# Optimization experiments

Measured on AMD Instinct MI355X. Metric: run time of the kernel, lower is better.

Reference implementation:

```python
import jax, jax.numpy as jnp
import numpy as np

N_EMBD = 1024
N_HEAD = 16
HEAD_DIM = N_EMBD // N_HEAD
WINDOW = 256
STRIDE = 128
GLOBAL = 16


def build_sparse_causal_mask(t):
    i = jnp.arange(t)[:, None]
    j = jnp.arange(t)[None, :]
    causal = j <= i
    allowed = causal & ((i - j) < WINDOW)
    allowed = allowed | (((i - j) % STRIDE == 0) & causal)
    allowed = allowed | ((j < GLOBAL) & causal)
    return allowed  # [t, t] bool


def setup_inputs() -> dict:
    key = jax.random.key(0)
    k1, k2, k3, k4, k5 = jax.random.split(key, 5)
    b, t = 2, 4096
    s = 1.0 / np.sqrt(N_EMBD)
    return {
        "x": jax.random.normal(k1, (b, t, N_EMBD), dtype=jnp.float32),
        "w_qkv": jax.random.normal(k2, (N_EMBD, 3 * N_EMBD), dtype=jnp.float32) * s,
        "b_qkv": jnp.zeros((3 * N_EMBD,), dtype=jnp.float32),
        "w_proj": jax.random.normal(k3, (N_EMBD, N_EMBD), dtype=jnp.float32) * s,
        "b_proj": jnp.zeros((N_EMBD,), dtype=jnp.float32),
    }


def reference(x, w_qkv, b_qkv, w_proj, b_proj):
    b, t, c = x.shape
    qkv = x @ w_qkv + b_qkv  # [b, t, 3c]
    q, k, v = jnp.split(qkv, 3, axis=2)
    # [b, h, t, d]
    q = q.reshape(b, t, N_HEAD, HEAD_DIM).transpose(0, 2, 1, 3)
    k = k.reshape(b, t, N_HEAD, HEAD_DIM).transpose(0, 2, 1, 3)
    v = v.reshape(b, t, N_HEAD, HEAD_DIM).transpose(0, 2, 1, 3)

    allowed = build_sparse_causal_mask(t)  # [t, t]
    scale = 1.0 / np.sqrt(HEAD_DIM)
    att = jnp.einsum("bhqd,bhkd->bhqk", q, k) * scale
    att = jnp.where(allowed, att, -jnp.inf)
    att = jax.nn.softmax(att, axis=-1)
    y = jnp.einsum("bhqk,bhkd->bhqd", att, v)
    y = y.transpose(0, 2, 1, 3).reshape(b, t, c)
    return y @ w_proj + b_proj
```

## Files before the change

kernel.cpp:

```cpp
#include <hip/hip_runtime.h>
#include <hip/hip_bf16.h>
#include <stdint.h>

typedef unsigned short ushort_t;
typedef __attribute__((ext_vector_type(8))) __bf16 bf16x8;
typedef __attribute__((ext_vector_type(8))) short short8;
typedef __attribute__((ext_vector_type(4))) float f32x4;
typedef __attribute__((ext_vector_type(4))) unsigned int uint4v;

__device__ __forceinline__ ushort_t f2b(float f) {
  union { float f; uint32_t u; } c; c.f = f;
  return (ushort_t)((c.u + 0x7fffu + ((c.u >> 16) & 1u)) >> 16);
}
__device__ __forceinline__ float b2f(ushort_t b) {
  union { float f; uint32_t u; } c; c.u = ((uint32_t)b) << 16;
  return c.f;
}
__device__ __forceinline__ float dot2bf(uint32_t qu, uint32_t ku, float acc) {
  union { uint32_t u; float f; } a, b, c, d;
  a.u = qu << 16; b.u = qu & 0xffff0000u;
  c.u = ku << 16; d.u = ku & 0xffff0000u;
  acc = fmaf(a.f, c.f, acc);
  return fmaf(b.f, d.f, acc);
}

__global__ __launch_bounds__(256) void f32_to_b16(
    const float* __restrict__ in, ushort_t* __restrict__ out) {
  const int i = (blockIdx.x * 256 + threadIdx.x) * 8;
  const f32x4 a = *(const f32x4*)&in[i];
  const f32x4 b = *(const f32x4*)&in[i + 4];
  short8 t;
#pragma unroll
  for (int j = 0; j < 4; j++) { t[j] = (short)f2b(a[j]); t[4 + j] = (short)f2b(b[j]); }
  *(short8*)&out[i] = t;
}

__global__ __launch_bounds__(256) void transpose_f2b(
    const float* __restrict__ in, ushort_t* __restrict__ out, int K, int N) {
  __shared__ __align__(16) ushort_t tile[64][72];
  const int k0 = blockIdx.x * 64, n0 = blockIdx.y * 64;
  const int tid = threadIdx.x;
#pragma unroll
  for (int i = 0; i < 4; i++) {
    const int idx = i * 256 + tid;
    const int r = idx >> 4, c = (idx & 15) * 4;
    const f32x4 a = *(const f32x4*)&in[(size_t)(k0 + r) * N + n0 + c];
#pragma unroll
    for (int j = 0; j < 4; j++) tile[r][c + j] = f2b(a[j]);
  }
  __syncthreads();
#pragma unroll
  for (int i = 0; i < 16; i++) {
    const int idx = i * 256 + tid;
    const int r = idx >> 6, c = idx & 63;
    out[(size_t)(n0 + r) * K + k0 + c] = tile[c][r];
  }
}

template <int MODE>
__global__ __launch_bounds__(256) void gemm_bt(
    const ushort_t* __restrict__ A, const ushort_t* __restrict__ Bt,
    const float* __restrict__ bias,
    ushort_t* __restrict__ q_out, ushort_t* __restrict__ k_out,
    ushort_t* __restrict__ v_out, float* __restrict__ f_out,
    int M, int N, int K) {
  __shared__ __align__(16) ushort_t Als[128 * 64];
  __shared__ __align__(16) ushort_t Bls[128 * 64];
  const int tid = threadIdx.x;
  const int wave = tid >> 6, lane = tid & 63;
  const int quad = lane >> 4, l15 = lane & 15;
  const int wr = wave >> 1, wc = wave & 1;
  const int linear = (int)blockIdx.x + (int)gridDim.x * (int)blockIdx.y;
  const int xcd = linear & 7, chunk = linear >> 3;
  const int by = xcd * 8 + (chunk & 7);
  const int bx = chunk >> 3;
  const int rowBase = by * 128;
  const int colBase = bx * 128;
  const f32x4 fzero = {0.f, 0.f, 0.f, 0.f};

  f32x4 acc[4][4];
#pragma unroll
  for (int mi = 0; mi < 4; mi++)
#pragma unroll
    for (int ni = 0; ni < 4; ni++) acc[mi][ni] = fzero;

  const int srow = tid >> 3;
  const int scol = (tid & 7) * 8;

  for (int kk = 0; kk < K; kk += 64) {
    __syncthreads();
#pragma unroll
    for (int s = 0; s < 4; s++) {
      const int r = s * 32 + srow;
      __builtin_amdgcn_global_load_lds(
          (const __attribute__((address_space(1))) unsigned int*)
              &A[(size_t)(rowBase + r) * K + kk + scol],
          (__attribute__((address_space(3))) unsigned int*)&Als[r * 64 + scol],
          16, 0, 0);
      __builtin_amdgcn_global_load_lds(
          (const __attribute__((address_space(1))) unsigned int*)
              &Bt[(size_t)(colBase + r) * K + kk + scol],
          (__attribute__((address_space(3))) unsigned int*)&Bls[r * 64 + scol],
          16, 0, 0);
    }
    __syncthreads();
#pragma unroll
    for (int ks = 0; ks < 2; ks++) {
      const int ko = ks * 32 + quad * 8;
      bf16x8 af[4], bfr[4];
#pragma unroll
      for (int mi = 0; mi < 4; mi++)
        af[mi] = *(const bf16x8*)&Als[(wr * 64 + mi * 16 + l15) * 64 + ko];
#pragma unroll
      for (int ni = 0; ni < 4; ni++)
        bfr[ni] = *(const bf16x8*)&Bls[(wc * 64 + ni * 16 + l15) * 64 + ko];
#pragma unroll
      for (int mi = 0; mi < 4; mi++)
#pragma unroll
        for (int ni = 0; ni < 4; ni++)
          acc[mi][ni] = __builtin_amdgcn_mfma_f32_16x16x32_bf16(
              af[mi], bfr[ni], acc[mi][ni], 0, 0, 0);
    }
  }

  if (MODE == 0) {
    const int which = colBase >> 10;
    ushort_t* dst = which == 0 ? q_out : (which == 1 ? k_out : v_out);
    const int h = ((colBase & 1023) >> 6) + wc;
#pragma unroll
    for (int mi = 0; mi < 4; mi++) {
#pragma unroll
      for (int ni = 0; ni < 4; ni++) {
        const int d = ni * 16 + l15;
        const float bv = bias[colBase + wc * 64 + d];
#pragma unroll
        for (int r = 0; r < 4; r++) {
          const int row = rowBase + wr * 64 + mi * 16 + quad * 4 + r;
          const int bidx = row >> 12, t = row & 4095;
          dst[(size_t)((bidx * 16 + h) * 4096 + t) * 64 + d] =
              f2b(acc[mi][ni][r] + bv);
        }
      }
    }
  } else {
#pragma unroll
    for (int mi = 0; mi < 4; mi++) {
#pragma unroll
      for (int ni = 0; ni < 4; ni++) {
        const int col = colBase + wc * 64 + ni * 16 + l15;
        const float bv = bias[col];
#pragma unroll
        for (int r = 0; r < 4; r++) {
          const int row = rowBase + wr * 64 + mi * 16 + quad * 4 + r;
          f_out[(size_t)row * N + col] = acc[mi][ni][r] + bv;
        }
      }
    }
  }
}

#define LP 72
__global__ __launch_bounds__(256) void sparse_attn(
    const ushort_t* __restrict__ Qb, const ushort_t* __restrict__ Kb,
    const ushort_t* __restrict__ Vb, ushort_t* __restrict__ Y) {
  __shared__ __align__(16) ushort_t Qls[64 * LP];
  __shared__ __align__(16) char smem[(64 * LP + 64 * LP + 4 * 16 * LP) * 2];
  ushort_t* Kls = (ushort_t*)smem;
  ushort_t* Vtls = Kls + 64 * LP;
  ushort_t* Pls = Vtls + 64 * LP;

  const int tid = threadIdx.x;
  const int wave = tid >> 6, lane = tid & 63;
  const int quad = lane >> 4, l15 = lane & 15;
  const int qt = (int)gridDim.x - 1 - (int)blockIdx.x;
  const int h = blockIdx.y, b = blockIdx.z;
  const int q0 = qt * 64;
  const size_t headoff = (size_t)(b * 16 + h) * 4096 * 64;
  const ushort_t* Qp = Qb + headoff;
  const ushort_t* Kp = Kb + headoff;
  const ushort_t* Vp = Vb + headoff;
  const f32x4 fzero = {0.f, 0.f, 0.f, 0.f};
  const float scale = 0.125f;

#pragma unroll
  for (int i = 0; i < 2; i++) {
    const int idx = i * 256 + tid;
    const int r = idx >> 3, c = (idx & 7) * 8;
    *(short8*)&Qls[r * LP + c] = *(const short8*)&Qp[(size_t)(q0 + r) * 64 + c];
  }
  __syncthreads();
  bf16x8 qf[2];
#pragma unroll
  for (int ks = 0; ks < 2; ks++)
    qf[ks] = *(const bf16x8*)&Qls[(wave * 16 + l15) * LP + ks * 32 + quad * 8];

  f32x4 o[4];
#pragma unroll
  for (int dt = 0; dt < 4; dt++) o[dt] = fzero;
  float mrun[4], lsum[4];
#pragma unroll
  for (int r = 0; r < 4; r++) { mrun[r] = -1e30f; lsum[r] = 0.f; }
  ushort_t* Pw = &Pls[wave * 16 * LP];

  auto dense_tile = [&](int k0, int mode) {
    __syncthreads();
#pragma unroll
    for (int i = 0; i < 2; i++) {
      const int idx = i * 256 + tid;
      const int r = idx >> 3, c = (idx & 7) * 8;
      *(short8*)&Kls[r * LP + c] = *(const short8*)&Kp[(size_t)(k0 + r) * 64 + c];
    }
#pragma unroll
    for (int i = 0; i < 2; i++) {
      const int idx = i * 256 + tid;
      const int key = idx & 63, dblk = (idx >> 6) * 8;
      short8 vv = *(const short8*)&Vp[(size_t)(k0 + key) * 64 + dblk];
#pragma unroll
      for (int m = 0; m < 8; m++) Vtls[(dblk + m) * LP + key] = (ushort_t)vv[m];
    }
    __syncthreads();

    f32x4 sacc[4];
#pragma unroll
    for (int ni = 0; ni < 4; ni++) sacc[ni] = fzero;
#pragma unroll
    for (int ks = 0; ks < 2; ks++) {
      const int ko = ks * 32 + quad * 8;
#pragma unroll
      for (int ni = 0; ni < 4; ni++) {
        bf16x8 kf = *(const bf16x8*)&Kls[(ni * 16 + l15) * LP + ko];
        sacc[ni] = __builtin_amdgcn_mfma_f32_16x16x32_bf16(qf[ks], kf, sacc[ni], 0, 0, 0);
      }
    }

    float p[4][4];
    const int i0 = q0 + wave * 16 + quad * 4;
    if (mode == 0) {
#pragma unroll
      for (int ni = 0; ni < 4; ni++)
#pragma unroll
        for (int r = 0; r < 4; r++) p[ni][r] = sacc[ni][r] * scale;
    } else {
#pragma unroll
      for (int ni = 0; ni < 4; ni++) {
        const int j = k0 + ni * 16 + l15;
#pragma unroll
        for (int r = 0; r < 4; r++) {
          const int dist = i0 + r - j;
          bool ok;
          if (mode == 1)      ok = dist >= 0;
          else if (mode == 2) ok = (dist < 256) || ((dist & 127) == 0);
          else                ok = (dist >= 0) &&
                                   ((dist < 256) || ((dist & 127) == 0) || (j < 16));
          p[ni][r] = ok ? sacc[ni][r] * scale : -1e30f;
        }
      }
    }

    float alpha[4];
#pragma unroll
    for (int r = 0; r < 4; r++) {
      float m = fmaxf(fmaxf(p[0][r], p[1][r]), fmaxf(p[2][r], p[3][r]));
      m = fmaxf(m, __shfl_xor(m, 1));
      m = fmaxf(m, __shfl_xor(m, 2));
      m = fmaxf(m, __shfl_xor(m, 4));
      m = fmaxf(m, __shfl_xor(m, 8));
      const float mnew = fmaxf(mrun[r], m);
      alpha[r] = __expf(mrun[r] - mnew);
      mrun[r] = mnew;
      float rs = 0.f;
#pragma unroll
      for (int ni = 0; ni < 4; ni++) {
        const float e = __expf(p[ni][r] - mnew);
        p[ni][r] = e;
        rs += e;
      }
      rs += __shfl_xor(rs, 1);
      rs += __shfl_xor(rs, 2);
      rs += __shfl_xor(rs, 4);
      rs += __shfl_xor(rs, 8);
      lsum[r] = lsum[r] * alpha[r] + rs;
    }
#pragma unroll
    for (int dt = 0; dt < 4; dt++)
#pragma unroll
      for (int r = 0; r < 4; r++) o[dt][r] *= alpha[r];

#pragma unroll
    for (int ni = 0; ni < 4; ni++)
#pragma unroll
      for (int r = 0; r < 4; r++)
        Pw[(quad * 4 + r) * LP + ni * 16 + l15] = f2b(p[ni][r]);
    __syncthreads();

#pragma unroll
    for (int ks = 0; ks < 2; ks++) {
      const int ko = ks * 32 + quad * 8;
      bf16x8 pf = *(const bf16x8*)&Pw[l15 * LP + ko];
#pragma unroll
      for (int dt = 0; dt < 4; dt++) {
        bf16x8 vf = *(const bf16x8*)&Vtls[(dt * 16 + l15) * LP + ko];
        o[dt] = __builtin_amdgcn_mfma_f32_16x16x32_bf16(pf, vf, o[dt], 0, 0, 0);
      }
    }
  };

  if (qt < 6) {
    for (int kt = 0; kt <= qt; kt++) dense_tile(kt * 64, 3);
  } else {
    dense_tile(0, 3);
    dense_tile((qt - 4) * 64, 2);
    dense_tile((qt - 3) * 64, 0);
    dense_tile((qt - 2) * 64, 0);
    dense_tile((qt - 1) * 64, 0);
    dense_tile(qt * 64, 1);

    const int rowl = wave * 16 + l15;
    const uint4v qv0 = *(const uint4v*)&Qls[rowl * LP + quad * 16];
    const uint4v qv1 = *(const uint4v*)&Qls[rowl * LP + quad * 16 + 8];
    const ushort_t* Kr = Kp + (size_t)rowl * 64 + quad * 16;
    const ushort_t* Vr = Vp + (size_t)rowl * 64 + quad * 16;

    float ms = -1e30f, ls = 0.f;
    f32x4 os4[4];
#pragma unroll
    for (int c = 0; c < 4; c++) os4[c] = fzero;

    auto sproc = [&](uint4v ka0, uint4v ka1, uint4v va0, uint4v va1) {
      float sd = 0.f;
#pragma unroll
      for (int m2 = 0; m2 < 4; m2++) {
        sd = dot2bf(qv0[m2], ka0[m2], sd);
        sd = dot2bf(qv1[m2], ka1[m2], sd);
      }
      sd += __shfl_xor(sd, 16);
      sd += __shfl_xor(sd, 32);
      const float sig = sd * scale;
      const float mnew = fmaxf(ms, sig);
      const float al = __expf(ms - mnew);
      const float e = __expf(sig - mnew);
      ms = mnew;
      ls = ls * al + e;
#pragma unroll
      for (int m2 = 0; m2 < 4; m2++) {
        union { uint32_t u; float f; } va, vb, vc, vd;
        va.u = va0[m2] << 16;
        vb.u = va0[m2] & 0xffff0000u;
        vc.u = va1[m2] << 16;
        vd.u = va1[m2] & 0xffff0000u;
        const int d0 = 2 * m2, d1 = 2 * m2 + 1;
        os4[d0 >> 2][d0 & 3] = fmaf(os4[d0 >> 2][d0 & 3], al, e * va.f);
        os4[d1 >> 2][d1 & 3] = fmaf(os4[d1 >> 2][d1 & 3], al, e * vb.f);
        os4[(d0 + 8) >> 2][d0 & 3] = fmaf(os4[(d0 + 8) >> 2][d0 & 3], al, e * vc.f);
        os4[(d1 + 8) >> 2][d1 & 3] = fmaf(os4[(d1 + 8) >> 2][d1 & 3], al, e * vd.f);
      }
    };

    int k0s = q0 - 384;
    if (k0s >= 64) {
      uint4v ka0 = *(const uint4v*)(Kr + (size_t)k0s * 64);
      uint4v ka1 = *(const uint4v*)(Kr + (size_t)k0s * 64 + 8);
      uint4v va0 = *(const uint4v*)(Vr + (size_t)k0s * 64);
      uint4v va1 = *(const uint4v*)(Vr + (size_t)k0s * 64 + 8);
      while (true) {
        const int nxt = k0s - 128;
        uint4v kb0, kb1, vb0, vb1;
        if (nxt >= 64) {
          kb0 = *(const uint4v*)(Kr + (size_t)nxt * 64);
          kb1 = *(const uint4v*)(Kr + (size_t)nxt * 64 + 8);
          vb0 = *(const uint4v*)(Vr + (size_t)nxt * 64);
          vb1 = *(const uint4v*)(Vr + (size_t)nxt * 64 + 8);
        }
        sproc(ka0, ka1, va0, va1);
        if (nxt < 64) break;
        ka0 = kb0; ka1 = kb1; va0 = vb0; va1 = vb1;
        k0s = nxt;
      }
    }

    __syncthreads();
    float* scr = (float*)smem + wave * (16 * 68);
#pragma unroll
    for (int c = 0; c < 4; c++)
      *(f32x4*)&scr[l15 * 68 + quad * 16 + c * 4] = os4[c];
    asm volatile("s_waitcnt lgkmcnt(0)" ::: "memory");
    __builtin_amdgcn_wave_barrier();
#pragma unroll
    for (int r = 0; r < 4; r++) {
      const float ms_r = __shfl(ms, quad * 4 + r);
      const float ls_r = __shfl(ls, quad * 4 + r);
      const float M = fmaxf(mrun[r], ms_r);
      const float ea = __expf(mrun[r] - M);
      const float eb = __expf(ms_r - M);
      lsum[r] = lsum[r] * ea + ls_r * eb;
#pragma unroll
      for (int dt = 0; dt < 4; dt++)
        o[dt][r] = o[dt][r] * ea + scr[(quad * 4 + r) * 68 + dt * 16 + l15] * eb;
    }
  }

#pragma unroll
  for (int dt = 0; dt < 4; dt++) {
#pragma unroll
    for (int r = 0; r < 4; r++) {
      const int t = q0 + wave * 16 + quad * 4 + r;
      const int c = h * 64 + dt * 16 + l15;
      Y[(size_t)(b * 4096 + t) * 1024 + c] = f2b(o[dt][r] / lsum[r]);
    }
  }
}

static const void* by_size(void* const* d_in, const int* in_sizes, int n_in,
                           int want, int fallback_idx) {
  for (int i = 0; i < n_in; i++)
    if (in_sizes[i] == want) return d_in[i];
  return d_in[fallback_idx];
}

extern "C" void kernel_launch(void* const* d_in, const int* in_sizes, int n_in,
                              void* d_out, int out_size, void* d_ws,
                              size_t ws_size, hipStream_t stream) {
  const float* x      = (const float*)by_size(d_in, in_sizes, n_in, 8388608, 0);
  const float* w_qkv  = (const float*)by_size(d_in, in_sizes, n_in, 3145728, 1);
  const float* b_qkv  = (const float*)by_size(d_in, in_sizes, n_in, 3072, 2);
  const float* w_proj = (const float*)by_size(d_in, in_sizes, n_in, 1048576, 3);
  const float* b_proj = (const float*)by_size(d_in, in_sizes, n_in, 1024, 4);
  float* out = (float*)d_out;
  char* ws = (char*)d_ws;
  ushort_t* wqkvT  = (ushort_t*)(ws);
  ushort_t* wprojT = (ushort_t*)(ws + 6291456);
  ushort_t* qb     = (ushort_t*)(ws + 8388608);
  ushort_t* kb     = (ushort_t*)(ws + 25165824);
  ushort_t* vb     = (ushort_t*)(ws + 41943040);
  ushort_t* yb     = (ushort_t*)(ws + 58720256);
  ushort_t* xb     = yb;

  if (ws_size < 75497472) return;

  f32_to_b16<<<4096, 256, 0, stream>>>(x, xb);
  transpose_f2b<<<dim3(16, 48), 256, 0, stream>>>(w_qkv, wqkvT, 1024, 3072);
  transpose_f2b<<<dim3(16, 16), 256, 0, stream>>>(w_proj, wprojT, 1024, 1024);
  gemm_bt<0><<<dim3(24, 64), 256, 0, stream>>>(
      xb, wqkvT, b_qkv, qb, kb, vb, nullptr, 8192, 3072, 1024);
  sparse_attn<<<dim3(64, 16, 2), 256, 0, stream>>>(qb, kb, vb, yb);
  gemm_bt<1><<<dim3(8, 64), 256, 0, stream>>>(
      yb, wprojT, b_proj, nullptr, nullptr, nullptr, out, 8192, 1024, 1024);
}
```

Before: 343.6 us.

## Process two query tiles per 512-thread block sharing K/V tiles, with XCD-aware mapping

Each attention block now covers two adjacent 64-row query tiles using 8 waves, so every loaded K/V key tile (and its V transpose) in LDS serves both tiles, cutting global and LDS fill traffic. Tiles that only one half needs are skipped per wave group through a mode of -1. Block indices are also remapped so each XCD handles a fixed set of batch-heads, which is meant to improve L2 locality. The trade-offs are a larger LDS footprint, half as many blocks, and some waves sitting idle at barriers on tiles they do not use. The parts of the sparse strided loop that are not shown must also be correct for the new row indexing.

Measured after the change: 302.6 us. -11.9%, faster.

```diff
diff --git a/kernel.cpp b/kernel.cpp
--- a/kernel.cpp
+++ b/kernel.cpp
@@ -160,11 +160,11 @@
 }
 
 #define LP 72
-__global__ __launch_bounds__(256) void sparse_attn(
+__global__ __launch_bounds__(512) void sparse_attn(
     const ushort_t* __restrict__ Qb, const ushort_t* __restrict__ Kb,
     const ushort_t* __restrict__ Vb, ushort_t* __restrict__ Y) {
-  __shared__ __align__(16) ushort_t Qls[64 * LP];
-  __shared__ __align__(16) char smem[(64 * LP + 64 * LP + 4 * 16 * LP) * 2];
+  __shared__ __align__(16) ushort_t Qls[128 * LP];
+  __shared__ __align__(16) char smem[(64 * LP + 64 * LP + 128 * LP) * 2];
   ushort_t* Kls = (ushort_t*)smem;
   ushort_t* Vtls = Kls + 64 * LP;
   ushort_t* Pls = Vtls + 64 * LP;
@@ -172,10 +172,16 @@
   const int tid = threadIdx.x;
   const int wave = tid >> 6, lane = tid & 63;
   const int quad = lane >> 4, l15 = lane & 15;
-  const int qt = (int)gridDim.x - 1 - (int)blockIdx.x;
-  const int h = blockIdx.y, b = blockIdx.z;
-  const int q0 = qt * 64;
-  const size_t headoff = (size_t)(b * 16 + h) * 4096 * 64;
+  const int wq = wave >> 2, wl = wave & 3;
+
+  const int linear = (int)blockIdx.x + 32 * (int)blockIdx.y + 512 * (int)blockIdx.z;
+  const int xcd = linear & 7, slot = linear >> 3;
+  const int pr = xcd * 4 + (slot & 3);
+  const int q0t = 2 * (31 - (slot >> 2));
+  const int q1t = q0t + 1;
+  const int h = pr & 15, b = pr >> 4;
+  const int q0 = (q0t + wq) * 64;
+  const size_t headoff = (size_t)pr * 4096 * 64;
   const ushort_t* Qp = Qb + headoff;
   const ushort_t* Kp = Kb + headoff;
   const ushort_t* Vp = Vb + headoff;
@@ -184,15 +190,15 @@
 
 #pragma unroll
   for (int i = 0; i < 2; i++) {
-    const int idx = i * 256 + tid;
+    const int idx = i * 512 + tid;
     const int r = idx >> 3, c = (idx & 7) * 8;
-    *(short8*)&Qls[r * LP + c] = *(const short8*)&Qp[(size_t)(q0 + r) * 64 + c];
+    *(short8*)&Qls[r * LP + c] = *(const short8*)&Qp[(size_t)(q0t * 64 + r) * 64 + c];
   }
   __syncthreads();
   bf16x8 qf[2];
 #pragma unroll
   for (int ks = 0; ks < 2; ks++)
-    qf[ks] = *(const bf16x8*)&Qls[(wave * 16 + l15) * LP + ks * 32 + quad * 8];
+    qf[ks] = *(const bf16x8*)&Qls[(wq * 64 + wl * 16 + l15) * LP + ks * 32 + quad * 8];
 
   f32x4 o[4];
 #pragma unroll
@@ -202,122 +208,126 @@
   for (int r = 0; r < 4; r++) { mrun[r] = -1e30f; lsum[r] = 0.f; }
   ushort_t* Pw = &Pls[wave * 16 * LP];
 
-  auto dense_tile = [&](int k0, int mode) {
-    __syncthreads();
-#pragma unroll
-    for (int i = 0; i < 2; i++) {
-      const int idx = i * 256 + tid;
-      const int r = idx >> 3, c = (idx & 7) * 8;
+  auto dense_tile = [&](int k0, int modeA, int modeB) {
+    const int mode = (wq == 0) ? modeA : modeB;
+    __syncthreads();
+    {
+      const int r = tid >> 3, c = (tid & 7) * 8;
       *(short8*)&Kls[r * LP + c] = *(const short8*)&Kp[(size_t)(k0 + r) * 64 + c];
     }
-#pragma unroll
-    for (int i = 0; i < 2; i++) {
-      const int idx = i * 256 + tid;
-      const int key = idx & 63, dblk = (idx >> 6) * 8;
+    {
+      const int key = tid & 63, dblk = (tid >> 6) * 8;
       short8 vv = *(const short8*)&Vp[(size_t)(k0 + key) * 64 + dblk];
 #pragma unroll
       for (int m = 0; m < 8; m++) Vtls[(dblk + m) * LP + key] = (ushort_t)vv[m];
     }
     __syncthreads();
 
-    f32x4 sacc[4];
-#pragma unroll
-    for (int ni = 0; ni < 4; ni++) sacc[ni] = fzero;
-#pragma unroll
-    for (int ks = 0; ks < 2; ks++) {
-      const int ko = ks * 32 + quad * 8;
-#pragma unroll
-      for (int ni = 0; ni < 4; ni++) {
-        bf16x8 kf = *(const bf16x8*)&Kls[(ni * 16 + l15) * LP + ko];
-        sacc[ni] = __builtin_amdgcn_mfma_f32_16x16x32_bf16(qf[ks], kf, sacc[ni], 0, 0, 0);
-      }
-    }
-
     float p[4][4];
-    const int i0 = q0 + wave * 16 + quad * 4;
-    if (mode == 0) {
+    if (mode >= 0) {
+      f32x4 sacc[4];
+#pragma unroll
+      for (int ni = 0; ni < 4; ni++) sacc[ni] = fzero;
+#pragma unroll
+      for (int ks = 0; ks < 2; ks++) {
+        const int ko = ks * 32 + quad * 8;
+#pragma unroll
+        for (int ni = 0; ni < 4; ni++) {
+          bf16x8 kf = *(const bf16x8*)&Kls[(ni * 16 + l15) * LP + ko];
+          sacc[ni] = __builtin_amdgcn_mfma_f32_16x16x32_bf16(qf[ks], kf, sacc[ni], 0, 0, 0);
+        }
+      }
+
+      const int i0 = q0 + wl * 16 + quad * 4;
+      if (mode == 0) {
+#pragma unroll
+        for (int ni = 0; ni < 4; ni++)
+#pragma unroll
+          for (int r = 0; r < 4; r++) p[ni][r] = sacc[ni][r] * scale;
+      } else {
+#pragma unroll
+        for (int ni = 0; ni < 4; ni++) {
+          const int j = k0 + ni * 16 + l15;
+#pragma unroll
+          for (int r = 0; r < 4; r++) {
+            const int dist = i0 + r - j;
+            bool ok;
+            if (mode == 1)      ok = dist >= 0;
+            else if (mode == 2) ok = (dist < 256) || ((dist & 127) == 0);
+            else                ok = (dist >= 0) &&
+                                     ((dist < 256) || ((dist & 127) == 0) || (j < 16));
+            p[ni][r] = ok ? sacc[ni][r] * scale : -1e30f;
+          }
+        }
+      }
+
+      float alpha[4];
+#pragma unroll
+      for (int r = 0; r < 4; r++) {
+        float m = fmaxf(fmaxf(p[0][r], p[1][r]), fmaxf(p[2][r], p[3][r]));
+        m = fmaxf(m, __shfl_xor(m, 1));
+        m = fmaxf(m, __shfl_xor(m, 2));
+        m = fmaxf(m, __shfl_xor(m, 4));
+        m = fmaxf(m, __shfl_xor(m, 8));
+        const float mnew = fmaxf(mrun[r], m);
+        alpha[r] = __expf(mrun[r] - mnew);
+        mrun[r] = mnew;
+        float rs = 0.f;
+#pragma unroll
+        for (int ni = 0; ni < 4; ni++) {
+          const float e = __expf(p[ni][r] - mnew);
+          p[ni][r] = e;
+          rs += e;
+        }
+        rs += __shfl_xor(rs, 1);
+        rs += __shfl_xor(rs, 2);
+        rs += __shfl_xor(rs, 4);
+        rs += __shfl_xor(rs, 8);
+        lsum[r] = lsum[r] * alpha[r] + rs;
+      }
+#pragma unroll
+      for (int dt = 0; dt < 4; dt++)
+#pragma unroll
+        for (int r = 0; r < 4; r++) o[dt][r] *= alpha[r];
+
 #pragma unroll
       for (int ni = 0; ni < 4; ni++)
 #pragma unroll
-        for (int r = 0; r < 4; r++) p[ni][r] = sacc[ni][r] * scale;
-    } else {
-#pragma unroll
-      for (int ni = 0; ni < 4; ni++) {
-        const int j = k0 + ni * 16 + l15;
-#pragma unroll
-        for (int r = 0; r < 4; r++) {
-          const int dist = i0 + r - j;
-          bool ok;
-          if (mode == 1)      ok = dist >= 0;
-          else if (mode == 2) ok = (dist < 256) || ((dist & 127) == 0);
-          else                ok = (dist >= 0) &&
-                                   ((dist < 256) || ((dist & 127) == 0) || (j < 16));
-          p[ni][r] = ok ? sacc[ni][r] * scale : -1e30f;
-        }
-      }
-    }
-
-    float alpha[4];
-#pragma unroll
-    for (int r = 0; r < 4; r++) {
-      float m = fmaxf(fmaxf(p[0][r], p[1][r]), fmaxf(p[2][r], p[3][r]));
-      m = fmaxf(m, __shfl_xor(m, 1));
-      m = fmaxf(m, __shfl_xor(m, 2));
-      m = fmaxf(m, __shfl_xor(m, 4));
-      m = fmaxf(m, __shfl_xor(m, 8));
-      const float mnew = fmaxf(mrun[r], m);
-      alpha[r] = __expf(mrun[r] - mnew);
-      mrun[r] = mnew;
-      float rs = 0.f;
-#pragma unroll
-      for (int ni = 0; ni < 4; ni++) {
-        const float e = __expf(p[ni][r] - mnew);
-        p[ni][r] = e;
-        rs += e;
-      }
-      rs += __shfl_xor(rs, 1);
-      rs += __shfl_xor(rs, 2);
-      rs += __shfl_xor(rs, 4);
-      rs += __shfl_xor(rs, 8);
-      lsum[r] = lsum[r] * alpha[r] + rs;
-    }
-#pragma unroll
-    for (int dt = 0; dt < 4; dt++)
-#pragma unroll
-      for (int r = 0; r < 4; r++) o[dt][r] *= alpha[r];
-
-#pragma unroll
-    for (int ni = 0; ni < 4; ni++)
-#pragma unroll
-      for (int r = 0; r < 4; r++)
-        Pw[(quad * 4 + r) * LP + ni * 16 + l15] = f2b(p[ni][r]);
-    __syncthreads();
-
-#pragma unroll
-    for (int ks = 0; ks < 2; ks++) {
-      const int ko = ks * 32 + quad * 8;
-      bf16x8 pf = *(const bf16x8*)&Pw[l15 * LP + ko];
-#pragma unroll
-      for (int dt = 0; dt < 4; dt++) {
-        bf16x8 vf = *(const bf16x8*)&Vtls[(dt * 16 + l15) * LP + ko];
-        o[dt] = __builtin_amdgcn_mfma_f32_16x16x32_bf16(pf, vf, o[dt], 0, 0, 0);
+        for (int r = 0; r < 4; r++)
+          Pw[(quad * 4 + r) * LP + ni * 16 + l15] = f2b(p[ni][r]);
+    }
+    __syncthreads();
+
+    if (mode >= 0) {
+#pragma unroll
+      for (int ks = 0; ks < 2; ks++) {
+        const int ko = ks * 32 + quad * 8;
+        bf16x8 pf = *(const bf16x8*)&Pw[l15 * LP + ko];
+#pragma unroll
+        for (int dt = 0; dt < 4; dt++) {
+          bf16x8 vf = *(const bf16x8*)&Vtls[(dt * 16 + l15) * LP + ko];
+          o[dt] = __builtin_amdgcn_mfma_f32_16x16x32_bf16(pf, vf, o[dt], 0, 0, 0);
+        }
       }
     }
   };
 
-  if (qt < 6) {
-    for (int kt = 0; kt <= qt; kt++) dense_tile(kt * 64, 3);
+  if (q1t < 6) {
+    for (int kt = 0; kt <= q1t; kt++)
+      dense_tile(kt * 64, kt <= q0t ? 3 : -1, 3);
   } else {
-    dense_tile(0, 3);
-    dense_tile((qt - 4) * 64, 2);
-    dense_tile((qt - 3) * 64, 0);
-    dense_tile((qt - 2) * 64, 0);
-    dense_tile((qt - 1) * 64, 0);
-    dense_tile(qt * 64, 1);
-
-    const int rowl = wave * 16 + l15;
-    const uint4v qv0 = *(const uint4v*)&Qls[rowl * LP + quad * 16];
-    const uint4v qv1 = *(const uint4v*)&Qls[rowl * LP + quad * 16 + 8];
+    dense_tile(0, 3, 3);
+    for (int kt = q0t - 4; kt <= q0t + 1; kt++) {
+      const int mA = (kt == q0t - 4) ? 2
+                   : (kt < q0t) ? 0 : (kt == q0t) ? 1 : -1;
+      const int mB = (kt == q0t - 4) ? -1
+                   : (kt == q0t - 3) ? 2 : (kt <= q0t) ? 0 : 1;
+      dense_tile(kt * 64, mA, mB);
+    }
+
+    const int rowl = wl * 16 + l15;
+    const uint4v qv0 = *(const uint4v*)&Qls[(wq * 64 + rowl) * LP + quad * 16];
+    const uint4v qv1 = *(const uint4v*)&Qls[(wq * 64 + rowl) * LP + quad * 16 + 8];
     const ushort_t* Kr = Kp + (size_t)rowl * 64 + quad * 16;
     const ushort_t* Vr = Vp + (size_t)rowl * 64 + quad * 16;
 
@@ -403,7 +413,7 @@
   for (int dt = 0; dt < 4; dt++) {
 #pragma unroll
     for (int r = 0; r < 4; r++) {
-      const int t = q0 + wave * 16 + quad * 4 + r;
+      const int t = q0 + wl * 16 + quad * 4 + r;
       const int c = h * 64 + dt * 16 + l15;
       Y[(size_t)(b * 4096 + t) * 1024 + c] = f2b(o[dt][r] / lsum[r]);
     }
@@ -442,7 +452,7 @@
   transpose_f2b<<<dim3(16, 16), 256, 0, stream>>>(w_proj, wprojT, 1024, 1024);
   gemm_bt<0><<<dim3(24, 64), 256, 0, stream>>>(
       xb, wqkvT, b_qkv, qb, kb, vb, nullptr, 8192, 3072, 1024);
-  sparse_attn<<<dim3(64, 16, 2), 256, 0, stream>>>(qb, kb, vb, yb);
+  sparse_attn<<<dim3(32, 16, 2), 512, 0, stream>>>(qb, kb, vb, yb);
   gemm_bt<1><<<dim3(8, 64), 256, 0, stream>>>(
       yb, wprojT, b_proj, nullptr, nullptr, nullptr, out, 8192, 1024, 1024);
 }
```
